# Kernel optimization log

Measured on AMD Instinct MI355X. Metric: run time of the kernel, lower is better.

Reference implementation:

```python
import jax, jax.numpy as jnp
import numpy as np
import math

B, T, D = 2, 2048, 1024
H, NL, DF = 16, 6, 4096
HD = D // H
EPS = 1e-5

def layer_norm(x, w, b):
    mu = jnp.mean(x, axis=-1, keepdims=True)
    var = jnp.mean((x - mu) ** 2, axis=-1, keepdims=True)
    return (x - mu) * jax.lax.rsqrt(var + EPS) * w + b

def setup_inputs() -> dict:
    key = jax.random.key(0)
    ks = jax.random.split(key, 12)
    def w(k, shape, scale=0.02):
        return jax.random.normal(k, shape, dtype=jnp.float32) * scale
    inp = {
        'sequences': jax.random.normal(ks[0], (B, T, D), dtype=jnp.float32),
        'Wq': w(ks[1], (NL, D, D)), 'bq': jnp.zeros((NL, D), jnp.float32),
        'Wk': w(ks[2], (NL, D, D)), 'bk': jnp.zeros((NL, D), jnp.float32),
        'Wv': w(ks[3], (NL, D, D)), 'bv': jnp.zeros((NL, D), jnp.float32),
        'Wo': w(ks[4], (NL, D, D)), 'bo': jnp.zeros((NL, D), jnp.float32),
        'Wz': w(ks[5], (NL, D, D)), 'bz': jnp.zeros((NL, D), jnp.float32),
        'Wr': w(ks[6], (NL, D, D)), 'br': jnp.zeros((NL, D), jnp.float32),
        'W1': w(ks[7], (NL, D, DF)), 'b1': jnp.zeros((NL, DF), jnp.float32),
        'W2': w(ks[8], (NL, DF, D)), 'b2': jnp.zeros((NL, D), jnp.float32),
        'ln1_w': jnp.ones((NL, D), jnp.float32), 'ln1_b': jnp.zeros((NL, D), jnp.float32),
        'ln2_w': jnp.ones((NL, D), jnp.float32), 'ln2_b': jnp.zeros((NL, D), jnp.float32),
        'lnf_w': jnp.ones((D,), jnp.float32), 'lnf_b': jnp.zeros((D,), jnp.float32),
    }
    return inp

def reference(sequences, Wq, bq, Wk, bk, Wv, bv, Wo, bo, Wz, bz, Wr, br,
              W1, b1, W2, b2, ln1_w, ln1_b, ln2_w, ln2_b, lnf_w, lnf_b):
    scale = 1.0 / math.sqrt(HD)
    causal = jnp.tril(jnp.ones((T, T), dtype=bool))  # mask[L:L+T, :L+T] with L=0
    x = sequences
    src = x
    for i in range(NL):
        xn = layer_norm(x, ln1_w[i], ln1_b[i])
        # QKV -> [B, H, T, HD]
        q = (xn @ Wq[i] + bq[i]).reshape(B, T, H, HD).transpose(0, 2, 1, 3)
        k = (xn @ Wk[i] + bk[i]).reshape(B, T, H, HD).transpose(0, 2, 1, 3)
        v = (xn @ Wv[i] + bv[i]).reshape(B, T, H, HD).transpose(0, 2, 1, 3)
        att = jnp.einsum('bhqd,bhkd->bhqk', q, k) * scale
        att = jnp.where(causal, att, -jnp.inf)
        att = jax.nn.softmax(att, axis=-1)
        y = jnp.einsum('bhqk,bhkd->bhqd', att, v)
        y = y.transpose(0, 2, 1, 3).reshape(B, T, D)
        x_attn = y @ Wo[i] + bo[i]
        z = jax.nn.sigmoid(xn @ Wz[i] + bz[i])
        r = jax.nn.sigmoid(xn @ Wr[i] + br[i])
        h_tilde = jnp.tanh(r * x_attn)
        x = (1.0 - z) * x + z * h_tilde
        xm = layer_norm(x, ln2_w[i], ln2_b[i])
        mlp = jax.nn.gelu(xm @ W1[i] + b1[i], approximate=False) @ W2[i] + b2[i]
        x = (1.0 - z) * x + z * mlp
        x = x + src
    x = layer_norm(x, lnf_w, lnf_b)
    return x
```

## Files before the change

### kernel.cpp

```cpp
#include <hip/hip_runtime.h>
#include <hip/hip_bf16.h>
#include <math.h>

#define B_ 2
#define T_ 2048
#define D_ 1024
#define H_ 16
#define NL_ 6
#define DF_ 4096
#define HD_ 64
#define M_ (B_*T_)

typedef __bf16 bf16;
typedef __attribute__((ext_vector_type(8))) __bf16 bf16x8;
typedef __attribute__((ext_vector_type(4))) float f32x4;
typedef __attribute__((ext_vector_type(16))) float f32x16;
typedef __attribute__((ext_vector_type(4))) unsigned u32x4;

#define BAR() __builtin_amdgcn_s_barrier()
#define LGKM0() asm volatile("s_waitcnt lgkmcnt(0)" ::: "memory")
#define VMC(n) asm volatile("s_waitcnt vmcnt(" #n ")" ::: "memory")

__device__ __forceinline__ void gload_lds16(const void* g, void* l) {
    __builtin_amdgcn_global_load_lds((const __attribute__((address_space(1))) void*)g,
                                     (__attribute__((address_space(3))) void*)l, 16, 0, 0);
}

__device__ __forceinline__ unsigned pk2(float a, float b) {
    bf16 lo = (bf16)a, hb = (bf16)b;
    return (unsigned)__builtin_bit_cast(unsigned short, lo) |
           ((unsigned)__builtin_bit_cast(unsigned short, hb) << 16);
}

__device__ __forceinline__ float4 ld4bf(const bf16* p) {
    float4 o;
    o.x = (float)p[0]; o.y = (float)p[1]; o.z = (float)p[2]; o.w = (float)p[3];
    return o;
}

template<bool OUT_BF16>
__global__ __launch_bounds__(256) void ln_kernel(const float* __restrict__ x,
        const float* __restrict__ w, const float* __restrict__ b,
        void* __restrict__ out) {
    const int row = blockIdx.x;
    const int t = threadIdx.x;
    const float4 xv = *(const float4*)(x + (long)row * D_ + t * 4);
    float s  = xv.x + xv.y + xv.z + xv.w;
    float sq = xv.x*xv.x + xv.y*xv.y + xv.z*xv.z + xv.w*xv.w;
    #pragma unroll
    for (int m = 32; m; m >>= 1) { s += __shfl_xor(s, m); sq += __shfl_xor(sq, m); }
    __shared__ float red[8];
    const int wid = t >> 6, lid = t & 63;
    if (lid == 0) { red[wid] = s; red[wid + 4] = sq; }
    __syncthreads();
    s  = red[0] + red[1] + red[2] + red[3];
    sq = red[4] + red[5] + red[6] + red[7];
    const float mu   = s * (1.0f / D_);
    const float var  = sq * (1.0f / D_) - mu * mu;
    const float rstd = rsqrtf(var + 1e-5f);
    const float4 wv = *(const float4*)(w + t * 4);
    const float4 bv = *(const float4*)(b + t * 4);
    float o0 = (xv.x - mu) * rstd * wv.x + bv.x;
    float o1 = (xv.y - mu) * rstd * wv.y + bv.y;
    float o2 = (xv.z - mu) * rstd * wv.z + bv.z;
    float o3 = (xv.w - mu) * rstd * wv.w + bv.w;
    if (OUT_BF16) {
        bf16* o = (bf16*)out + (long)row * D_ + t * 4;
        o[0] = (bf16)o0; o[1] = (bf16)o1; o[2] = (bf16)o2; o[3] = (bf16)o3;
    } else {
        float* o = (float*)out + (long)row * D_ + t * 4;
        o[0] = o0; o[1] = o1; o[2] = o2; o[3] = o3;
    }
}

__global__ __launch_bounds__(256) void wconv_all(
        const float* __restrict__ Wq, const float* __restrict__ Wk,
        const float* __restrict__ Wv, const float* __restrict__ Wz,
        const float* __restrict__ Wr, const float* __restrict__ Wo,
        const float* __restrict__ W1, const float* __restrict__ W2,
        bf16* __restrict__ wt) {
    __shared__ float s[32][33];
    const int bid = blockIdx.x;
    const float* src; bf16* dst; int t, K, nlg;
    if (bid < 6144) {
        const int m = bid >> 10; t = bid & 1023; K = 1024; nlg = 5;
        switch (m) {
            case 0: src = Wq; dst = wt; break;
            case 1: src = Wk; dst = wt + (1u << 20); break;
            case 2: src = Wv; dst = wt + (2u << 20); break;
            case 3: src = Wz; dst = wt + (3u << 20); break;
            case 4: src = Wr; dst = wt + (4u << 20); break;
            default: src = Wo; dst = wt + (5u << 20); break;
        }
    } else if (bid < 10240) {
        t = bid - 6144; K = 1024; nlg = 7; src = W1; dst = wt + (6u << 20);
    } else {
        t = bid - 10240; K = 4096; nlg = 5; src = W2; dst = wt + (10u << 20);
    }
    const int N = 1 << (nlg + 5);
    const int k0 = (t >> nlg) * 32, n0 = (t & ((1 << nlg) - 1)) * 32;
    const int c = threadIdx.x & 31, r8 = threadIdx.x >> 5;
    #pragma unroll
    for (int it = 0; it < 4; it++)
        s[r8 + it*8][c] = src[(long)(k0 + r8 + it*8) * N + n0 + c];
    __syncthreads();
    #pragma unroll
    for (int it = 0; it < 4; it++)
        dst[(long)(n0 + r8 + it*8) * K + k0 + c] = (bf16)s[c][r8 + it*8];
}

#define MFMA16(a, b, c) __builtin_amdgcn_mfma_f32_16x16x32_bf16(a, b, c, 0, 0, 0)
#define MFMA32(a, b, c) __builtin_amdgcn_mfma_f32_32x32x16_bf16(a, b, c, 0, 0, 0)

__device__ __forceinline__ void gemm128_core(const bf16* __restrict__ A, const bf16* __restrict__ Bt,
        const int Ks, const int NT, const int m0, const int n0, char* lds, f32x4 (&acc)[4][4]) {
    const int tid = threadIdx.x;
    const int lane = tid & 63, w = tid >> 6;
    const int wm = w >> 1, wn = w & 1;
    const int cl = lane & 15, gl = lane >> 4;
    const int srow = lane >> 2;
    const int sxc = (((lane & 3) ^ ((lane >> 3) & 3)) << 3);
    const bf16* pa0 = A  + (size_t)(m0 + w * 32 + srow) * Ks + sxc;
    const bf16* pa1 = pa0 + (size_t)16 * Ks;
    const bf16* pb  = Bt + (size_t)(n0 + w * 16 + srow) * Ks + sxc;
    char* laA = lds + w * 2048;
    char* laB = lds + 32768 + w * 1024;

#define STG(KT, BUF) do { \
    gload_lds16(pa0 + (size_t)(KT) * 32, laA + (BUF) * 16384); \
    gload_lds16(pa1 + (size_t)(KT) * 32, laA + (BUF) * 16384 + 1024); \
    gload_lds16(pb  + (size_t)(KT) * 32, laB + (BUF) * 8192); } while (0)

    STG(0, 0); STG(1, 1);
    VMC(3);

    const int xo  = ((gl ^ ((cl >> 1) & 3)) << 4);
    const int rdA = (wm * 64 + cl) * 64 + xo;
    const int rdB = (wn * 64 + cl) * 64 + xo;

    for (int kt = 0; kt < NT; ++kt) {
        const int buf = kt & 1;
        const char* sA = lds + buf * 16384;
        const char* sB = lds + 32768 + buf * 8192;
        BAR();
        bf16x8 a[4], b[4];
        #pragma unroll
        for (int mi = 0; mi < 4; mi++) a[mi] = *(const bf16x8*)(sA + rdA + mi * 1024);
        #pragma unroll
        for (int ni = 0; ni < 4; ni++) b[ni] = *(const bf16x8*)(sB + rdB + ni * 1024);
        LGKM0();
        BAR();
        if (kt + 2 < NT) STG(kt + 2, buf);
        __builtin_amdgcn_s_setprio(1);
        #pragma unroll
        for (int mi = 0; mi < 4; mi++)
            #pragma unroll
            for (int ni = 0; ni < 4; ni++)
                acc[mi][ni] = MFMA16(a[mi], b[ni], acc[mi][ni]);
        __builtin_amdgcn_s_setprio(0);
        if (kt + 2 < NT)      { VMC(3); }
        else if (kt + 1 < NT) { VMC(0); }
    }
#undef STG
}

__global__ __launch_bounds__(512, 4) void gemm5_k(const bf16* __restrict__ A, const bf16* __restrict__ Bt,
        const float* __restrict__ bq, const float* __restrict__ bk, const float* __restrict__ bvv,
        const float* __restrict__ bz, const float* __restrict__ br,
        bf16* __restrict__ oq, bf16* __restrict__ ok, bf16* __restrict__ ov,
        bf16* __restrict__ oz, bf16* __restrict__ orr) {
    __shared__ __align__(16) char lds[49152];
    int bid = blockIdx.x;
    bid = (bid & 7) * 80 + (bid >> 3);
    const int m0 = (bid / 40) * 256, n0 = (bid % 40) * 128;
    f32x4 acc[4][4];
    #pragma unroll
    for (int i = 0; i < 4; i++)
        #pragma unroll
        for (int j = 0; j < 4; j++) acc[i][j] = (f32x4){0.f, 0.f, 0.f, 0.f};
    gemm128_core(A, Bt, 1024, 32, m0, n0, lds, acc);
    const int tid = threadIdx.x, lane = tid & 63, w = tid >> 6;
    const int wm = w >> 1, wn = w & 1, cl = lane & 15, gl = lane >> 4;
    const int seg = n0 >> 10;
    const int lc0 = (n0 & 1023) + wn * 64;
    const float* bias; int mode; bf16* outp;
    switch (seg) {
        case 0:  bias = bq;  mode = 0; outp = oq;  break;
        case 1:  bias = bk;  mode = 0; outp = ok;  break;
        case 2:  bias = bvv; mode = 1; outp = ov;  break;
        case 3:  bias = bz;  mode = 2; outp = oz;  break;
        default: bias = br;  mode = 2; outp = orr; break;
    }
    const float scl = (seg == 0) ? 0.125f : 1.0f;
    #pragma unroll
    for (int mi = 0; mi < 4; mi++) {
        #pragma unroll
        for (int ni = 0; ni < 4; ni++) {
            const int lcol = lc0 + ni * 16 + cl;
            const float bv = bias[lcol];
            #pragma unroll
            for (int r = 0; r < 4; r++) {
                const int row = m0 + wm * 64 + mi * 16 + gl * 4 + r;
                const float v = (acc[mi][ni][r] + bv) * scl;
                if (mode == 0) {
                    outp[(long)row * 1024 + lcol] = (bf16)v;
                } else if (mode == 1) {
                    outp[((long)(row >> 11) * 1024 + lcol) * T_ + (row & 2047)] = (bf16)v;
                } else {
                    outp[(long)row * 1024 + lcol] = (bf16)(1.0f / (1.0f + __expf(-v)));
                }
            }
        }
    }
}

__global__ __launch_bounds__(512, 4) void gemmG_k(const bf16* __restrict__ A, const bf16* __restrict__ Bt,
        const float* __restrict__ bias, bf16* __restrict__ out) {
    __shared__ __align__(16) char lds[49152];
    int bid = blockIdx.x;
    bid = (bid & 7) * 64 + (bid >> 3);
    const int m0 = (bid >> 5) * 256, n0 = (bid & 31) * 128;
    f32x4 acc[4][4];
    #pragma unroll
    for (int i = 0; i < 4; i++)
        #pragma unroll
        for (int j = 0; j < 4; j++) acc[i][j] = (f32x4){0.f, 0.f, 0.f, 0.f};
    gemm128_core(A, Bt, 1024, 32, m0, n0, lds, acc);
    const int tid = threadIdx.x, lane = tid & 63, w = tid >> 6;
    const int wm = w >> 1, wn = w & 1, cl = lane & 15, gl = lane >> 4;
    #pragma unroll
    for (int mi = 0; mi < 4; mi++) {
        #pragma unroll
        for (int ni = 0; ni < 4; ni++) {
            const int col = n0 + wn * 64 + ni * 16 + cl;
            const float bv = bias[col];
            #pragma unroll
            for (int r = 0; r < 4; r++) {
                const int row = m0 + wm * 64 + mi * 16 + gl * 4 + r;
                float v = acc[mi][ni][r] + bv;
                v = 0.5f * v * (1.0f + erff(v * 0.70710678118f));
                out[(long)row * DF_ + col] = (bf16)v;
            }
        }
    }
}

__global__ __launch_bounds__(512, 4) void gemmP_k(const bf16* __restrict__ A, const bf16* __restrict__ Bt,
        bf16* __restrict__ p0, bf16* __restrict__ p1, bf16* __restrict__ p2, bf16* __restrict__ p3) {
    __shared__ __align__(16) char lds[49152];
    int bid = blockIdx.x;
    bid = (bid & 7) * 64 + (bid >> 3);
    const int mt = bid >> 5, s = (bid >> 3) & 3, ntl = bid & 7;
    const int m0 = mt * 256, n0 = ntl * 128;
    f32x4 acc[4][4];
    #pragma unroll
    for (int i = 0; i < 4; i++)
        #pragma unroll
        for (int j = 0; j < 4; j++) acc[i][j] = (f32x4){0.f, 0.f, 0.f, 0.f};
    gemm128_core(A + s * 1024, Bt + s * 1024, 4096, 32, m0, n0, lds, acc);
    bf16* outp = (s == 0) ? p0 : (s == 1) ? p1 : (s == 2) ? p2 : p3;
    const int tid = threadIdx.x, lane = tid & 63, w = tid >> 6;
    const int wm = w >> 1, wn = w & 1, cl = lane & 15, gl = lane >> 4;
    #pragma unroll
    for (int mi = 0; mi < 4; mi++) {
        #pragma unroll
        for (int ni = 0; ni < 4; ni++) {
            const int col = n0 + wn * 64 + ni * 16 + cl;
            #pragma unroll
            for (int r = 0; r < 4; r++) {
                const int row = m0 + wm * 64 + mi * 16 + gl * 4 + r;
                outp[(long)row * 1024 + col] = (bf16)acc[mi][ni][r];
            }
        }
    }
}

__global__ __launch_bounds__(512, 4) void gemmWoG_kernel(const bf16* __restrict__ A,
        const bf16* __restrict__ Bt, const float* __restrict__ bias,
        float* __restrict__ x, const bf16* __restrict__ z, const bf16* __restrict__ rr) {
    __shared__ __align__(16) char lds[49152];
    int bid = blockIdx.x;
    bid = (bid & 7) * 16 + (bid >> 3);
    const int m0 = (bid >> 3) * 256, n0 = (bid & 7) * 128;
    f32x4 acc[4][4];
    #pragma unroll
    for (int i = 0; i < 4; i++)
        #pragma unroll
        for (int j = 0; j < 4; j++) acc[i][j] = (f32x4){0.f, 0.f, 0.f, 0.f};
    gemm128_core(A, Bt, 1024, 32, m0, n0, lds, acc);
    const int tid = threadIdx.x, lane = tid & 63, w = tid >> 6;
    const int wm = w >> 1, wn = w & 1, cl = lane & 15, gl = lane >> 4;
    #pragma unroll
    for (int mi = 0; mi < 4; mi++) {
        #pragma unroll
        for (int ni = 0; ni < 4; ni++) {
            const int col = n0 + wn * 64 + ni * 16 + cl;
            const float bv = bias[col];
            #pragma unroll
            for (int r = 0; r < 4; r++) {
                const int row = m0 + wm * 64 + mi * 16 + gl * 4 + r;
                const long idx = (long)row * D_ + col;
                const float xa = acc[mi][ni][r] + bv;
                const float zv = (float)z[idx];
                const float ht = tanhf((float)rr[idx] * xa);
                x[idx] = (1.f - zv) * x[idx] + zv * ht;
            }
        }
    }
}

__global__ __launch_bounds__(256, 2) void attn_kernel(const bf16* __restrict__ q,
        const bf16* __restrict__ k, const bf16* __restrict__ vT,
        bf16* __restrict__ y) {
    __shared__ __align__(16) char lds[32768];
    const int tid = threadIdx.x, wid = tid >> 6, lane = tid & 63;
    const int col = lane & 31, hi = lane >> 5;
    const int bid = blockIdx.x;
    const int xcd = bid & 7, idx = bid >> 3;
    const int bh = xcd + 8 * (idx & 3);
    const int sg = idx >> 2;
    const int g = (sg & 1) ? (sg >> 1) : (15 - (sg >> 1));
    const int qt = 4 * g + wid;
    const int qb = qt * 32;
    const int b = bh >> 4, h = bh & 15;
    const int NP = 2 * g + 2;
    const int nt64 = (qt >> 1) + 1;

    const bf16* qB = q  + (size_t)b * T_ * D_ + h * HD_;
    const bf16* kB = k  + (size_t)b * T_ * D_ + h * HD_;
    const bf16* vB = vT + (size_t)b * D_ * T_ + (size_t)h * HD_ * T_;

    const int sr = wid * 8 + (lane >> 3);
    const int sc = lane & 7;
    const bf16* kS0 = kB + (size_t)sr * D_ + 8 * (sc ^ (sr & 7));
    const bf16* kS1 = kS0 + (size_t)32 * D_;
    const bf16* vS0 = vB + (size_t)sr * T_ + 8 * (sc ^ (sr & 7));
    const bf16* vS1 = vS0 + (size_t)32 * T_;
    char* dK = lds + wid * 1024;
    char* dV = lds + 16384 + wid * 1024;

#define ASTG(J, BUF) do { \
    const size_t ko_ = (size_t)(J) * 64 * D_; \
    const size_t vo_ = (size_t)(J) * 64; \
    gload_lds16(kS0 + ko_, dK + (BUF) * 8192); \
    gload_lds16(kS1 + ko_, dK + (BUF) * 8192 + 4096); \
    gload_lds16(vS0 + vo_, dV + (BUF) * 8192); \
    gload_lds16(vS1 + vo_, dV + (BUF) * 8192 + 4096); } while (0)

    bf16x8 qf0, qf1, qf2, qf3;
    {
        const bf16* qp = qB + (size_t)(qb + col) * D_ + 8 * hi;
        qf0 = *(const bf16x8*)(qp);
        qf1 = *(const bf16x8*)(qp + 16);
        qf2 = *(const bf16x8*)(qp + 32);
        qf3 = *(const bf16x8*)(qp + 48);
    }

    f32x16 Od0, Od1;
    #pragma unroll
    for (int i = 0; i < 16; i++) { Od0[i] = 0.f; Od1[i] = 0.f; }
    float mrun = -INFINITY, lrun = 0.f;

    ASTG(0, 0);
    ASTG(1, 1);
    VMC(4);
    BAR();

    const int swz = col & 7;
    for (int j = 0; j < NP; ++j) {
        const int buf = j & 1;
        if (j < nt64) {
            const char* bK = lds + buf * 8192;
            const char* bV = lds + 16384 + buf * 8192;
            bf16x8 kf0[4], kf1[4], vf0[4], vf1[4];
            #pragma unroll
            for (int cs = 0; cs < 4; cs++) {
                const int ch = ((hi + 2 * cs) ^ swz) * 16;
                kf0[cs] = *(const bf16x8*)(bK + col * 128 + ch);
                kf1[cs] = *(const bf16x8*)(bK + (col + 32) * 128 + ch);
                vf0[cs] = *(const bf16x8*)(bV + col * 128 + ch);
                vf1[cs] = *(const bf16x8*)(bV + (col + 32) * 128 + ch);
            }
            f32x16 S0, S1;
            #pragma unroll
            for (int i = 0; i < 16; i++) { S0[i] = 0.f; S1[i] = 0.f; }
            S0 = MFMA32(kf0[0], qf0, S0); S0 = MFMA32(kf0[1], qf1, S0);
            S0 = MFMA32(kf0[2], qf2, S0); S0 = MFMA32(kf0[3], qf3, S0);
            S1 = MFMA32(kf1[0], qf0, S1); S1 = MFMA32(kf1[1], qf1, S1);
            S1 = MFMA32(kf1[2], qf2, S1); S1 = MFMA32(kf1[3], qf3, S1);
            float p[32];
            #pragma unroll
            for (int r = 0; r < 16; r++) { p[r] = S0[r]; p[16 + r] = S1[r]; }
            if (j == nt64 - 1) {
                const int qr = qb + col;
                #pragma unroll
                for (int r = 0; r < 32; r++) {
                    const int kvl = 64 * j + 32 * (r >> 4)
                                  + (r & 3) + 8 * ((r & 15) >> 2) + 4 * hi;
                    if (kvl > qr) p[r] = -3.0e38f;
                }
            }
            float tm = p[0];
            #pragma unroll
            for (int r = 1; r < 32; r++) tm = fmaxf(tm, p[r]);
            tm = fmaxf(tm, __shfl_xor(tm, 32));
            if (!__all(tm <= mrun + 8.f)) {
                const float mn = fmaxf(mrun, tm);
                const float al = __expf(mrun - mn);
                lrun *= al;
                #pragma unroll
                for (int i = 0; i < 16; i++) { Od0[i] *= al; Od1[i] *= al; }
                mrun = mn;
            }
            float ts = 0.f;
            #pragma unroll
            for (int r = 0; r < 32; r++) { p[r] = __expf(p[r] - mrun); ts += p[r]; }
            ts += __shfl_xor(ts, 32);
            lrun += ts;
            bf16x8 pbf[4];
            #pragma unroll
            for (int t = 0; t < 2; t++) {
                const unsigned pw0 = pk2(p[16*t+0],  p[16*t+1]),  pw1 = pk2(p[16*t+2],  p[16*t+3]);
                const unsigned pw2 = pk2(p[16*t+4],  p[16*t+5]),  pw3 = pk2(p[16*t+6],  p[16*t+7]);
                const unsigned pw4 = pk2(p[16*t+8],  p[16*t+9]),  pw5 = pk2(p[16*t+10], p[16*t+11]);
                const unsigned pw6 = pk2(p[16*t+12], p[16*t+13]), pw7 = pk2(p[16*t+14], p[16*t+15]);
                const unsigned px0 = __shfl_xor((int)pw0, 32), px1 = __shfl_xor((int)pw1, 32);
                const unsigned px2 = __shfl_xor((int)pw2, 32), px3 = __shfl_xor((int)pw3, 32);
                const unsigned px4 = __shfl_xor((int)pw4, 32), px5 = __shfl_xor((int)pw5, 32);
                const unsigned px6 = __shfl_xor((int)pw6, 32), px7 = __shfl_xor((int)pw7, 32);
                const u32x4 c0 = hi ? (u32x4){px2, px3, pw2, pw3} : (u32x4){pw0, pw1, px0, px1};
                const u32x4 c1 = hi ? (u32x4){px6, px7, pw6, pw7} : (u32x4){pw4, pw5, px4, px5};
                pbf[2*t]   = __builtin_bit_cast(bf16x8, c0);
                pbf[2*t+1] = __builtin_bit_cast(bf16x8, c1);
            }
            #pragma unroll
            for (int f = 0; f < 4; f++) {
                Od0 = MFMA32(vf0[f], pbf[f], Od0);
                Od1 = MFMA32(vf1[f], pbf[f], Od1);
            }
        }
        BAR();
        if (j + 2 < NP) { ASTG(j + 2, buf); VMC(4); }
        else            { VMC(0); }
        BAR();
    }

    const float inv = 1.0f / lrun;
    bf16* yr = y + (size_t)(b * T_ + qb + col) * D_ + h * HD_;
    #pragma unroll
    for (int rg = 0; rg < 4; rg++) {
        const int d0 = 8 * rg + 4 * hi;
        uint2 s0 = { pk2(Od0[4*rg] * inv, Od0[4*rg+1] * inv), pk2(Od0[4*rg+2] * inv, Od0[4*rg+3] * inv) };
        *(uint2*)(yr + d0) = s0;
        uint2 s1 = { pk2(Od1[4*rg] * inv, Od1[4*rg+1] * inv), pk2(Od1[4*rg+2] * inv, Od1[4*rg+3] * inv) };
        *(uint2*)(yr + 32 + d0) = s1;
    }
#undef ASTG
}

template<bool LN>
__global__ __launch_bounds__(256) void gate2ln_kernel(float* __restrict__ x,
        const bf16* __restrict__ z,
        const bf16* __restrict__ p0, const bf16* __restrict__ p1,
        const bf16* __restrict__ p2, const bf16* __restrict__ p3,
        const float* __restrict__ src, const float* __restrict__ b2,
        const float* __restrict__ lw, const float* __restrict__ lb,
        bf16* __restrict__ xn) {
    const int row = blockIdx.x, t = threadIdx.x;
    const long i = (long)row * D_ + t * 4;
    float4 xv = *(const float4*)(x + i);
    const float4 zv = ld4bf(z + i);
    const float4 a0 = ld4bf(p0 + i);
    const float4 a1 = ld4bf(p1 + i);
    const float4 a2 = ld4bf(p2 + i);
    const float4 a3 = ld4bf(p3 + i);
    const float4 sv = *(const float4*)(src + i);
    const float4 bb = *(const float4*)(b2 + t * 4);
    xv.x = (1.f - zv.x) * xv.x + zv.x * (a0.x + a1.x + a2.x + a3.x + bb.x) + sv.x;
    xv.y = (1.f - zv.y) * xv.y + zv.y * (a0.y + a1.y + a2.y + a3.y + bb.y) + sv.y;
    xv.z = (1.f - zv.z) * xv.z + zv.z * (a0.z + a1.z + a2.z + a3.z + bb.z) + sv.z;
    xv.w = (1.f - zv.w) * xv.w + zv.w * (a0.w + a1.w + a2.w + a3.w + bb.w) + sv.w;
    *(float4*)(x + i) = xv;
    if (LN) {
        float s  = xv.x + xv.y + xv.z + xv.w;
        float sq = xv.x*xv.x + xv.y*xv.y + xv.z*xv.z + xv.w*xv.w;
        #pragma unroll
        for (int m = 32; m; m >>= 1) { s += __shfl_xor(s, m); sq += __shfl_xor(sq, m); }
        __shared__ float red[8];
        const int wid = t >> 6, lid = t & 63;
        if (lid == 0) { red[wid] = s; red[wid + 4] = sq; }
        __syncthreads();
        s  = red[0] + red[1] + red[2] + red[3];
        sq = red[4] + red[5] + red[6] + red[7];
        const float mu   = s * (1.0f / D_);
        const float var  = sq * (1.0f / D_) - mu * mu;
        const float rstd = rsqrtf(var + 1e-5f);
        const float4 wv = *(const float4*)(lw + t * 4);
        const float4 bv = *(const float4*)(lb + t * 4);
        bf16* o = xn + i;
        o[0] = (bf16)((xv.x - mu) * rstd * wv.x + bv.x);
        o[1] = (bf16)((xv.y - mu) * rstd * wv.y + bv.y);
        o[2] = (bf16)((xv.z - mu) * rstd * wv.z + bv.z);
        o[3] = (bf16)((xv.w - mu) * rstd * wv.w + bv.w);
    }
}

extern "C" void kernel_launch(void* const* d_in, const int* in_sizes, int n_in,
                              void* d_out, int out_size, void* d_ws, size_t ws_size,
                              hipStream_t stream) {
    const float* seq   = (const float*)d_in[0];
    const float* Wq    = (const float*)d_in[1];  const float* bq = (const float*)d_in[2];
    const float* Wk    = (const float*)d_in[3];  const float* bk = (const float*)d_in[4];
    const float* Wv    = (const float*)d_in[5];  const float* bv = (const float*)d_in[6];
    const float* Wo    = (const float*)d_in[7];  const float* bo = (const float*)d_in[8];
    const float* Wz    = (const float*)d_in[9];  const float* bz = (const float*)d_in[10];
    const float* Wr    = (const float*)d_in[11]; const float* br = (const float*)d_in[12];
    const float* W1    = (const float*)d_in[13]; const float* b1 = (const float*)d_in[14];
    const float* W2    = (const float*)d_in[15]; const float* b2 = (const float*)d_in[16];
    const float* ln1w  = (const float*)d_in[17]; const float* ln1b = (const float*)d_in[18];
    const float* ln2w  = (const float*)d_in[19]; const float* ln2b = (const float*)d_in[20];
    const float* lnfw  = (const float*)d_in[21]; const float* lnfb = (const float*)d_in[22];

    char* ws = (char*)d_ws;
    float* x   = (float*)(ws);
    bf16*  z   = (bf16*)(ws + ((size_t)16 << 20));
    bf16*  r   = (bf16*)(ws + ((size_t)32 << 20));
    bf16*  xa  = (bf16*)(ws + ((size_t)48 << 20));
    bf16*  xn  = (bf16*)(ws + ((size_t)64 << 20));
    bf16*  qb_ = (bf16*)(ws + ((size_t)72 << 20));
    bf16*  kb_ = (bf16*)(ws + ((size_t)80 << 20));
    bf16*  vtb = (bf16*)(ws + ((size_t)88 << 20));
    bf16*  yb  = (bf16*)(ws + ((size_t)96 << 20));
    bf16*  h1  = (bf16*)(ws + ((size_t)104 << 20));
    bf16*  wt  = (bf16*)(ws + ((size_t)136 << 20));
    bf16*  pt2 = (bf16*)(ws + ((size_t)172 << 20));
    bf16*  pt3 = (bf16*)(ws + ((size_t)188 << 20));

    bf16* wto = wt + (5u << 20);
    bf16* wt1 = wt + (6u << 20);
    bf16* wt2 = wt + (10u << 20);

    hipMemcpyAsync(x, seq, (size_t)M_ * D_ * 4, hipMemcpyDeviceToDevice, stream);

    for (int i = 0; i < NL_; i++) {
        const long dd = (long)i * D_ * D_;
        wconv_all<<<14336, 256, 0, stream>>>(Wq + dd, Wk + dd, Wv + dd, Wz + dd,
                                             Wr + dd, Wo + dd,
                                             W1 + (long)i * D_ * DF_,
                                             W2 + (long)i * DF_ * D_, wt);
        if (i == 0)
            ln_kernel<true><<<M_, 256, 0, stream>>>(x, ln1w, ln1b, xn);
        gemm5_k<<<640, 512, 0, stream>>>(xn, wt,
                bq + i * D_, bk + i * D_, bv + i * D_, bz + i * D_, br + i * D_,
                qb_, kb_, vtb, z, r);
        attn_kernel<<<512, 256, 0, stream>>>(qb_, kb_, vtb, yb);
        gemmWoG_kernel<<<128, 512, 0, stream>>>(yb, wto, bo + i * D_, x, z, r);
        ln_kernel<true><<<M_, 256, 0, stream>>>(x, ln2w + i * D_, ln2b + i * D_, xn);
        gemmG_k<<<512, 512, 0, stream>>>(xn, wt1, b1 + i * DF_, h1);
        gemmP_k<<<512, 512, 0, stream>>>(h1, wt2, xa, r, pt2, pt3);
        if (i + 1 < NL_)
            gate2ln_kernel<true><<<M_, 256, 0, stream>>>(x, z, xa, r, pt2, pt3, seq, b2 + i * D_,
                    ln1w + (i + 1) * D_, ln1b + (i + 1) * D_, xn);
        else
            gate2ln_kernel<false><<<M_, 256, 0, stream>>>(x, z, xa, r, pt2, pt3, seq, b2 + i * D_,
                    nullptr, nullptr, nullptr);
    }
    ln_kernel<false><<<M_, 256, 0, stream>>>(x, lnfw, lnfb, d_out);
}
```

Measured before the change: 1.703 ms.

## Use 256x256 tiles with a ping-pong pipelined core for MLP GEMMs

Adds a 256x256-tile GEMM core with K=64 steps, 128KB LDS double buffering, and loads and MFMAs interleaved across four phases separated by barriers. The MLP up-projection (GELU) and split-K down-projection kernels now use it, so each launch has half as many blocks. Larger tiles raise arithmetic intensity and cut global and LDS traffic per FLOP. In exchange, occupancy drops to 2 blocks per CU, register pressure rises with 128 accumulators per thread, and the grid shrinks to 256 blocks, which may leave some CUs unevenly loaded.

```diff
diff --git a/kernel.cpp b/kernel.cpp
--- a/kernel.cpp
+++ b/kernel.cpp
@@ -164,6 +164,117 @@
 #undef STG
 }
 
+__device__ __forceinline__ void gemm256_core(const bf16* __restrict__ A, const bf16* __restrict__ Bt,
+        const int Ks, const int NT, const int m0, const int n0, char* lds, f32x4 (&acc)[8][4]) {
+    const int tid = threadIdx.x;
+    const int lane = tid & 63, w = tid >> 6;
+    const int wm = w >> 2, wn = w & 3;
+    const int cl = lane & 15, gl = lane >> 4;
+    const int srow = lane >> 3;
+    const int scol = ((lane & 7) ^ srow) * 8;
+    const bf16* pa0 = A  + (size_t)(m0 + w * 16 + srow) * Ks + scol;
+    const bf16* pa1 = pa0 + (size_t)8 * Ks;
+    const bf16* pb0 = Bt + (size_t)(n0 + w * 16 + srow) * Ks + scol;
+    const bf16* pb1 = pb0 + (size_t)8 * Ks;
+    char* la = lds + w * 2048;
+    char* lb = lds + 65536 + w * 2048;
+    const size_t hA = (size_t)128 * Ks;
+
+#define STGA(H, KT, BUF) do { \
+    gload_lds16(pa0 + (size_t)(H) * hA + (size_t)(KT) * 64, la + (BUF) * 32768 + (H) * 16384); \
+    gload_lds16(pa1 + (size_t)(H) * hA + (size_t)(KT) * 64, la + (BUF) * 32768 + (H) * 16384 + 1024); } while (0)
+#define STGB(H, KT, BUF) do { \
+    gload_lds16(pb0 + (size_t)(H) * hA + (size_t)(KT) * 64, lb + (BUF) * 32768 + (H) * 16384); \
+    gload_lds16(pb1 + (size_t)(H) * hA + (size_t)(KT) * 64, lb + (BUF) * 32768 + (H) * 16384 + 1024); } while (0)
+
+    STGA(0, 0, 0); STGA(1, 0, 0); STGB(0, 0, 0); STGB(1, 0, 0);
+    STGB(0, 1, 1); STGA(0, 1, 1); STGA(1, 1, 1);
+    VMC(6);
+    BAR();
+
+    const int X0  = (gl * 16) ^ ((cl & 7) << 4);
+    const int rdA = (wm * 128 + cl) * 128 + X0;
+    const int rdB = (wn * 64  + cl) * 128 + X0;
+
+    for (int kt = 0; kt < NT; ++kt) {
+        const int buf = kt & 1;
+        const char* sAb = lds + buf * 32768;
+        const char* sBb = lds + 65536 + buf * 32768;
+        const bool st1 = (kt + 1 < NT), st2 = (kt + 2 < NT);
+        bf16x8 a0[4][2], a4[4][2], b01[2][2], b23[2][2];
+        #pragma unroll
+        for (int mi = 0; mi < 4; mi++) {
+            a0[mi][0] = *(const bf16x8*)(sAb + rdA + mi * 2048);
+            a0[mi][1] = *(const bf16x8*)(sAb + (rdA ^ 64) + mi * 2048);
+        }
+        #pragma unroll
+        for (int ni = 0; ni < 2; ni++) {
+            b01[ni][0] = *(const bf16x8*)(sBb + rdB + ni * 2048);
+            b01[ni][1] = *(const bf16x8*)(sBb + (rdB ^ 64) + ni * 2048);
+        }
+        if (st1) STGB(1, kt + 1, buf ^ 1);
+        BAR(); LGKM0();
+        __builtin_amdgcn_s_setprio(1);
+        #pragma unroll
+        for (int mi = 0; mi < 4; mi++)
+            #pragma unroll
+            for (int ni = 0; ni < 2; ni++) {
+                acc[mi][ni] = MFMA16(a0[mi][0], b01[ni][0], acc[mi][ni]);
+                acc[mi][ni] = MFMA16(a0[mi][1], b01[ni][1], acc[mi][ni]);
+            }
+        __builtin_amdgcn_s_setprio(0);
+        BAR();
+        #pragma unroll
+        for (int mi = 0; mi < 4; mi++) {
+            a4[mi][0] = *(const bf16x8*)(sAb + rdA + (mi + 4) * 2048);
+            a4[mi][1] = *(const bf16x8*)(sAb + (rdA ^ 64) + (mi + 4) * 2048);
+        }
+        BAR(); LGKM0();
+        __builtin_amdgcn_s_setprio(1);
+        #pragma unroll
+        for (int mi = 0; mi < 4; mi++)
+            #pragma unroll
+            for (int ni = 0; ni < 2; ni++) {
+                acc[mi + 4][ni] = MFMA16(a4[mi][0], b01[ni][0], acc[mi + 4][ni]);
+                acc[mi + 4][ni] = MFMA16(a4[mi][1], b01[ni][1], acc[mi + 4][ni]);
+            }
+        __builtin_amdgcn_s_setprio(0);
+        BAR();
+        #pragma unroll
+        for (int ni = 0; ni < 2; ni++) {
+            b23[ni][0] = *(const bf16x8*)(sBb + rdB + (ni + 2) * 2048);
+            b23[ni][1] = *(const bf16x8*)(sBb + (rdB ^ 64) + (ni + 2) * 2048);
+        }
+        if (st2) STGA(0, kt + 2, buf);
+        BAR(); LGKM0();
+        __builtin_amdgcn_s_setprio(1);
+        #pragma unroll
+        for (int mi = 0; mi < 4; mi++)
+            #pragma unroll
+            for (int ni = 0; ni < 2; ni++) {
+                acc[mi + 4][ni + 2] = MFMA16(a4[mi][0], b23[ni][0], acc[mi + 4][ni + 2]);
+                acc[mi + 4][ni + 2] = MFMA16(a4[mi][1], b23[ni][1], acc[mi + 4][ni + 2]);
+            }
+        __builtin_amdgcn_s_setprio(0);
+        BAR();
+        if (st2) { STGA(1, kt + 2, buf); STGB(0, kt + 2, buf); }
+        __builtin_amdgcn_s_setprio(1);
+        #pragma unroll
+        for (int mi = 0; mi < 4; mi++)
+            #pragma unroll
+            for (int ni = 0; ni < 2; ni++) {
+                acc[mi][ni + 2] = MFMA16(a0[mi][0], b23[ni][0], acc[mi][ni + 2]);
+                acc[mi][ni + 2] = MFMA16(a0[mi][1], b23[ni][1], acc[mi][ni + 2]);
+            }
+        __builtin_amdgcn_s_setprio(0);
+        if (st2)      { VMC(6); }
+        else if (st1) { VMC(0); }
+        BAR();
+    }
+#undef STGA
+#undef STGB
+}
+
 __global__ __launch_bounds__(512, 4) void gemm5_k(const bf16* __restrict__ A, const bf16* __restrict__ Bt,
         const float* __restrict__ bq, const float* __restrict__ bk, const float* __restrict__ bvv,
         const float* __restrict__ bz, const float* __restrict__ br,
@@ -214,29 +325,29 @@
     }
 }
 
-__global__ __launch_bounds__(512, 4) void gemmG_k(const bf16* __restrict__ A, const bf16* __restrict__ Bt,
+__global__ __launch_bounds__(512, 2) void gemmG8_k(const bf16* __restrict__ A, const bf16* __restrict__ Bt,
         const float* __restrict__ bias, bf16* __restrict__ out) {
-    __shared__ __align__(16) char lds[49152];
+    __shared__ __align__(16) char lds[131072];
     int bid = blockIdx.x;
-    bid = (bid & 7) * 64 + (bid >> 3);
-    const int m0 = (bid >> 5) * 256, n0 = (bid & 31) * 128;
-    f32x4 acc[4][4];
-    #pragma unroll
-    for (int i = 0; i < 4; i++)
+    bid = (bid & 7) * 32 + (bid >> 3);
+    const int m0 = (bid >> 4) * 256, n0 = (bid & 15) * 256;
+    f32x4 acc[8][4];
+    #pragma unroll
+    for (int i = 0; i < 8; i++)
         #pragma unroll
         for (int j = 0; j < 4; j++) acc[i][j] = (f32x4){0.f, 0.f, 0.f, 0.f};
-    gemm128_core(A, Bt, 1024, 32, m0, n0, lds, acc);
+    gemm256_core(A, Bt, 1024, 16, m0, n0, lds, acc);
     const int tid = threadIdx.x, lane = tid & 63, w = tid >> 6;
-    const int wm = w >> 1, wn = w & 1, cl = lane & 15, gl = lane >> 4;
-    #pragma unroll
-    for (int mi = 0; mi < 4; mi++) {
+    const int wm = w >> 2, wn = w & 3, cl = lane & 15, gl = lane >> 4;
+    #pragma unroll
+    for (int mi = 0; mi < 8; mi++) {
         #pragma unroll
         for (int ni = 0; ni < 4; ni++) {
             const int col = n0 + wn * 64 + ni * 16 + cl;
             const float bv = bias[col];
             #pragma unroll
             for (int r = 0; r < 4; r++) {
-                const int row = m0 + wm * 64 + mi * 16 + gl * 4 + r;
+                const int row = m0 + wm * 128 + mi * 16 + gl * 4 + r;
                 float v = acc[mi][ni][r] + bv;
                 v = 0.5f * v * (1.0f + erff(v * 0.70710678118f));
                 out[(long)row * DF_ + col] = (bf16)v;
@@ -245,30 +356,31 @@
     }
 }
 
-__global__ __launch_bounds__(512, 4) void gemmP_k(const bf16* __restrict__ A, const bf16* __restrict__ Bt,
+__global__ __launch_bounds__(512, 2) void gemmP8_k(const bf16* __restrict__ A, const bf16* __restrict__ Bt,
         bf16* __restrict__ p0, bf16* __restrict__ p1, bf16* __restrict__ p2, bf16* __restrict__ p3) {
-    __shared__ __align__(16) char lds[49152];
+    __shared__ __align__(16) char lds[131072];
     int bid = blockIdx.x;
-    bid = (bid & 7) * 64 + (bid >> 3);
-    const int mt = bid >> 5, s = (bid >> 3) & 3, ntl = bid & 7;
-    const int m0 = mt * 256, n0 = ntl * 128;
-    f32x4 acc[4][4];
-    #pragma unroll
-    for (int i = 0; i < 4; i++)
+    bid = (bid & 7) * 32 + (bid >> 3);
+    const int mt = bid >> 4, rest = bid & 15;
+    const int nt = rest >> 2, s = rest & 3;
+    const int m0 = mt * 256, n0 = nt * 256;
+    f32x4 acc[8][4];
+    #pragma unroll
+    for (int i = 0; i < 8; i++)
         #pragma unroll
         for (int j = 0; j < 4; j++) acc[i][j] = (f32x4){0.f, 0.f, 0.f, 0.f};
-    gemm128_core(A + s * 1024, Bt + s * 1024, 4096, 32, m0, n0, lds, acc);
+    gemm256_core(A + s * 1024, Bt + s * 1024, 4096, 16, m0, n0, lds, acc);
     bf16* outp = (s == 0) ? p0 : (s == 1) ? p1 : (s == 2) ? p2 : p3;
     const int tid = threadIdx.x, lane = tid & 63, w = tid >> 6;
-    const int wm = w >> 1, wn = w & 1, cl = lane & 15, gl = lane >> 4;
-    #pragma unroll
-    for (int mi = 0; mi < 4; mi++) {
+    const int wm = w >> 2, wn = w & 3, cl = lane & 15, gl = lane >> 4;
+    #pragma unroll
+    for (int mi = 0; mi < 8; mi++) {
         #pragma unroll
         for (int ni = 0; ni < 4; ni++) {
             const int col = n0 + wn * 64 + ni * 16 + cl;
             #pragma unroll
             for (int r = 0; r < 4; r++) {
-                const int row = m0 + wm * 64 + mi * 16 + gl * 4 + r;
+                const int row = m0 + wm * 128 + mi * 16 + gl * 4 + r;
                 outp[(long)row * 1024 + col] = (bf16)acc[mi][ni][r];
             }
         }
@@ -556,8 +668,8 @@
         attn_kernel<<<512, 256, 0, stream>>>(qb_, kb_, vtb, yb);
         gemmWoG_kernel<<<128, 512, 0, stream>>>(yb, wto, bo + i * D_, x, z, r);
         ln_kernel<true><<<M_, 256, 0, stream>>>(x, ln2w + i * D_, ln2b + i * D_, xn);
-        gemmG_k<<<512, 512, 0, stream>>>(xn, wt1, b1 + i * DF_, h1);
-        gemmP_k<<<512, 512, 0, stream>>>(h1, wt2, xa, r, pt2, pt3);
+        gemmG8_k<<<256, 512, 0, stream>>>(xn, wt1, b1 + i * DF_, h1);
+        gemmP8_k<<<256, 512, 0, stream>>>(h1, wt2, xa, r, pt2, pt3);
         if (i + 1 < NL_)
             gate2ln_kernel<true><<<M_, 256, 0, stream>>>(x, z, xa, r, pt2, pt3, seq, b2 + i * D_,
                     ln1w + (i + 1) * D_, ln1b + (i + 1) * D_, xn);
```

New measurement: 1.705 ms. No clear change (+0.1%).
